# Performance work log

Measured on AMD Instinct MI355X. Metric: run time of the kernel, lower is better.

Reference implementation:

```python
import jax, jax.numpy as jnp
import numpy as np

TOP_K = 2

def setup_inputs() -> dict:
    key = jax.random.key(0)
    ks = jax.random.split(key, 6)
    B, S, D, H, E = 2, 1024, 512, 1024, 8
    x = jax.random.normal(ks[0], (B, S, D), dtype=jnp.float32)
    w_router = jax.random.normal(ks[1], (E, D), dtype=jnp.float32) / np.sqrt(D)
    b_router = jnp.zeros((E,), dtype=jnp.float32)
    w1 = jax.random.normal(ks[2], (E, H, D), dtype=jnp.float32) / np.sqrt(D)   # per-expert fc1 (hidden, in)
    w2 = jax.random.normal(ks[3], (E, D, H), dtype=jnp.float32) / np.sqrt(H)   # per-expert fc2 (out, hidden)
    return {"x": x, "w_router": w_router, "b_router": b_router, "w1": w1, "w2": w2}


def reference(x, w_router, b_router, w1, w2):
    B, S, D = x.shape
    E = w_router.shape[0]
    x_flat = x.reshape(-1, D)                                  # [T, D]
    # Router: logits -> softmax -> top-k -> renormalize -> dispatch weights
    router_logits = x_flat @ w_router.T + b_router             # [T, E]
    probs = jax.nn.softmax(router_logits, axis=-1)
    top_p, top_i = jax.lax.top_k(probs, TOP_K)                 # [T, K]
    top_p = top_p / jnp.sum(top_p, axis=-1, keepdims=True)
    # dispatch[t, e] = normalized prob if e in top-k of t else 0
    dispatch = jnp.sum(jax.nn.one_hot(top_i, E, dtype=x.dtype) * top_p[..., None], axis=1)  # [T, E]
    # Dense-masked expert MLP (mathematically identical to gather/GEMM/scatter):
    h = jax.nn.gelu(jnp.einsum('td,ehd->teh', x_flat, w1), approximate=False)  # [T, E, H]
    y = jnp.einsum('teh,edh->ted', h, w2)                      # [T, E, Dout]
    out = jnp.einsum('ted,te->td', y, dispatch)                # weighted combine
    out = out.reshape(B, S, -1)
    return out, router_logits
```

## Files before the change

kernel.cpp:

```cpp
#include <hip/hip_runtime.h>
#include <hip/hip_bf16.h>
#include <math.h>

#define T_TOK 2048
#define DIM 512
#define HID 1024
#define NE 8
#define CAP 1024

#define ROUT_BLKS 128
#define CAST_BLKS 2048

typedef __attribute__((ext_vector_type(8))) short short8;
typedef __attribute__((ext_vector_type(4))) float floatx4;

__device__ __forceinline__ unsigned short f2bf_bits(float f) {
    __hip_bfloat16 h = __float2bfloat16(f);
    return *reinterpret_cast<unsigned short*>(&h);
}

__device__ __forceinline__ void gl2lds(const unsigned short* g, unsigned short* l) {
    __builtin_amdgcn_global_load_lds(
        (const __attribute__((address_space(1))) unsigned int*)g,
        (__attribute__((address_space(3))) unsigned int*)l, 16, 0, 0);
}

__device__ __forceinline__ short8 frag(const unsigned short* s, int row, int kg) {
    return *reinterpret_cast<const short8*>(s + row * 128 + (((kg) ^ (row & 7)) << 3));
}

template<int T>
__device__ __forceinline__ void stage_tile(const unsigned short* src, size_t RS,
                                           int k0, unsigned short* lds,
                                           int wave, int lane) {
    int ro = lane >> 4, gr = lane & 15;
#pragma unroll
    for (int i = wave; i < T / 4; i += 4) {
        int r = i * 4 + ro;
        gl2lds(src + (size_t)r * RS + k0 + (((gr ^ (r & 7)) << 3)),
               lds + i * 512);
    }
}

__global__ __launch_bounds__(256)
void prep(const float* __restrict__ x, const float* __restrict__ wr,
          const float* __restrict__ br,
          const float* __restrict__ w1, const float* __restrict__ w2,
          unsigned short* __restrict__ w1b, unsigned short* __restrict__ w2b,
          unsigned short* __restrict__ xg, int* __restrict__ counts,
          int2* __restrict__ pairSlot, float2* __restrict__ pw,
          float* __restrict__ logits_out) {
    int bx = blockIdx.x;
    int tid = threadIdx.x;
    if (bx >= ROUT_BLKS) {
        const int n1 = NE * HID * DIM / 4;
        int base = (bx - ROUT_BLKS) * 1024 + tid;
#pragma unroll
        for (int rep = 0; rep < 4; rep++) {
            int i = base + rep * 256;
            const float* s = (i < n1) ? w1 : w2;
            unsigned short* d = (i < n1) ? w1b : w2b;
            int j = (i < n1) ? i : i - n1;
            float4 v = reinterpret_cast<const float4*>(s)[j];
            ushort4 o;
            o.x = f2bf_bits(v.x); o.y = f2bf_bits(v.y);
            o.z = f2bf_bits(v.z); o.w = f2bf_bits(v.w);
            reinterpret_cast<ushort4*>(d)[j] = o;
        }
        return;
    }
    int wave = tid >> 6, lane = tid & 63;
    for (int it = 0; it < 4; it++) {
        int t = bx * 16 + it * 4 + wave;
        const float4* xr = reinterpret_cast<const float4*>(x + (size_t)t * DIM);
        float4 xa = xr[lane * 2], xc = xr[lane * 2 + 1];
        short8 o;
        o[0] = (short)f2bf_bits(xa.x); o[1] = (short)f2bf_bits(xa.y);
        o[2] = (short)f2bf_bits(xa.z); o[3] = (short)f2bf_bits(xa.w);
        o[4] = (short)f2bf_bits(xc.x); o[5] = (short)f2bf_bits(xc.y);
        o[6] = (short)f2bf_bits(xc.z); o[7] = (short)f2bf_bits(xc.w);
        float p[NE];
#pragma unroll
        for (int e = 0; e < NE; e++) {
            const float4* wre = reinterpret_cast<const float4*>(wr + e * DIM);
            float4 wa = wre[lane * 2], wc = wre[lane * 2 + 1];
            p[e] = xa.x * wa.x + xa.y * wa.y + xa.z * wa.z + xa.w * wa.w
                 + xc.x * wc.x + xc.y * wc.y + xc.z * wc.z + xc.w * wc.w;
        }
#pragma unroll
        for (int e = 0; e < NE; e++) {
#pragma unroll
            for (int off = 32; off >= 1; off >>= 1)
                p[e] += __shfl_xor(p[e], off, 64);
        }
        int slot1 = 0, slot2 = 0;
        if (lane == 0) {
            float l[NE];
#pragma unroll
            for (int e = 0; e < NE; e++) {
                l[e] = p[e] + br[e];
                logits_out[(size_t)t * NE + e] = l[e];
            }
            int e1 = 0;
#pragma unroll
            for (int e = 1; e < NE; e++) if (l[e] > l[e1]) e1 = e;
            int es = -1;
#pragma unroll
            for (int e = 0; e < NE; e++) {
                if (e == e1) continue;
                if (es < 0 || l[e] > l[es]) es = e;
            }
            float z = expf(l[es] - l[e1]);
            float inv = 1.f / (1.f + z);
            int pos1 = atomicAdd(&counts[e1 * 16], 1);
            if (pos1 > CAP - 1) pos1 = CAP - 1;
            int pos2 = atomicAdd(&counts[es * 16], 1);
            if (pos2 > CAP - 1) pos2 = CAP - 1;
            slot1 = e1 * CAP + pos1;
            slot2 = es * CAP + pos2;
            pairSlot[t] = make_int2(slot1, slot2);
            pw[t] = make_float2(inv, z * inv);
        }
        slot1 = __shfl(slot1, 0);
        slot2 = __shfl(slot2, 0);
        *reinterpret_cast<short8*>(xg + (size_t)slot1 * DIM + lane * 8) = o;
        *reinterpret_cast<short8*>(xg + (size_t)slot2 * DIM + lane * 8) = o;
    }
}

__global__ __launch_bounds__(256, 3)
void gemm1(const unsigned short* __restrict__ xg,
           const unsigned short* __restrict__ w1b,
           const int* __restrict__ counts,
           unsigned short* __restrict__ Hb) {
    int bx = blockIdx.x;
    int e = bx & 7;
    int rest = bx >> 3;
    int n0 = (rest & 7) * 128;
    int m0 = (rest >> 3) * 64;
    int cnt = counts[e * 16]; if (cnt > CAP) cnt = CAP;
    if (m0 >= cnt) return;

    __shared__ __align__(16) unsigned short s_a[64 * 128];
    __shared__ __align__(16) unsigned short s_b[128 * 128];

    int tid = threadIdx.x, wave = tid >> 6, lane = tid & 63;
    int g = lane >> 4, ln = lane & 15;
    int wm = wave & 1, wn = wave >> 1;

    const unsigned short* asrc = xg + (size_t)(e * CAP + m0) * DIM;
    const unsigned short* bsrc = w1b + (size_t)(e * HID + n0) * DIM;

    floatx4 acc[2][4];
#pragma unroll
    for (int mf = 0; mf < 2; mf++)
#pragma unroll
        for (int nf = 0; nf < 4; nf++) acc[mf][nf] = (floatx4){0.f, 0.f, 0.f, 0.f};

    for (int ph = 0; ph < 4; ph++) {
        int k0 = ph * 128;
        stage_tile<64>(asrc, DIM, k0, s_a, wave, lane);
        stage_tile<128>(bsrc, DIM, k0, s_b, wave, lane);
        __syncthreads();
#pragma unroll
        for (int ks = 0; ks < 4; ks++) {
            short8 a0 = frag(s_a, wm * 32 + ln, ks * 4 + g);
            short8 a1 = frag(s_a, wm * 32 + 16 + ln, ks * 4 + g);
#pragma unroll
            for (int nf = 0; nf < 4; nf++) {
                short8 b = frag(s_b, wn * 64 + nf * 16 + ln, ks * 4 + g);
                acc[0][nf] = __builtin_amdgcn_mfma_f32_16x16x32_bf16(a0, b, acc[0][nf], 0, 0, 0);
                acc[1][nf] = __builtin_amdgcn_mfma_f32_16x16x32_bf16(a1, b, acc[1][nf], 0, 0, 0);
            }
        }
        __syncthreads();
    }
#pragma unroll
    for (int mf = 0; mf < 2; mf++)
#pragma unroll
        for (int nf = 0; nf < 4; nf++)
#pragma unroll
            for (int r = 0; r < 4; r++) {
                int lr = wm * 32 + mf * 16 + g * 4 + r;
                int col = n0 + wn * 64 + nf * 16 + ln;
                float v = acc[mf][nf][r];
                float gv = 0.5f * v * (1.f + erff(v * 0.70710678118f));
                Hb[(size_t)(e * CAP + m0 + lr) * HID + col] = f2bf_bits(gv);
            }
}

__global__ __launch_bounds__(256, 3)
void gemm2(const unsigned short* __restrict__ Hb,
           const unsigned short* __restrict__ w2b,
           const int* __restrict__ counts,
           float* __restrict__ ybuf) {
    int bx = blockIdx.x;
    int e = bx & 7;
    int rest = bx >> 3;
    int n0 = (rest & 3) * 128;
    int kv = (rest >> 2) & 1;
    int m0 = (rest >> 3) * 64;
    int cnt = counts[e * 16]; if (cnt > CAP) cnt = CAP;
    if (m0 >= cnt) return;

    __shared__ __align__(16) unsigned short s_a[64 * 128];
    __shared__ __align__(16) unsigned short s_b[128 * 128];

    int tid = threadIdx.x, wave = tid >> 6, lane = tid & 63;
    int g = lane >> 4, ln = lane & 15;
    int wm = wave & 1, wn = wave >> 1;

    const unsigned short* asrc = Hb + (size_t)(e * CAP + m0) * HID;
    const unsigned short* bsrc = w2b + (size_t)(e * DIM + n0) * HID;

    floatx4 acc[2][4];
#pragma unroll
    for (int mf = 0; mf < 2; mf++)
#pragma unroll
        for (int nf = 0; nf < 4; nf++) acc[mf][nf] = (floatx4){0.f, 0.f, 0.f, 0.f};

    for (int ph = 0; ph < 4; ph++) {
        int k0 = kv * 512 + ph * 128;
        stage_tile<64>(asrc, HID, k0, s_a, wave, lane);
        stage_tile<128>(bsrc, HID, k0, s_b, wave, lane);
        __syncthreads();
#pragma unroll
        for (int ks = 0; ks < 4; ks++) {
            short8 a0 = frag(s_a, wm * 32 + ln, ks * 4 + g);
            short8 a1 = frag(s_a, wm * 32 + 16 + ln, ks * 4 + g);
#pragma unroll
            for (int nf = 0; nf < 4; nf++) {
                short8 b = frag(s_b, wn * 64 + nf * 16 + ln, ks * 4 + g);
                acc[0][nf] = __builtin_amdgcn_mfma_f32_16x16x32_bf16(a0, b, acc[0][nf], 0, 0, 0);
                acc[1][nf] = __builtin_amdgcn_mfma_f32_16x16x32_bf16(a1, b, acc[1][nf], 0, 0, 0);
            }
        }
        __syncthreads();
    }
    float* yb = ybuf + (size_t)kv * (NE * CAP * DIM);
#pragma unroll
    for (int mf = 0; mf < 2; mf++)
#pragma unroll
        for (int nf = 0; nf < 4; nf++)
#pragma unroll
            for (int r = 0; r < 4; r++) {
                int lr = wm * 32 + mf * 16 + g * 4 + r;
                int col = n0 + wn * 64 + nf * 16 + ln;
                yb[(size_t)(e * CAP + m0 + lr) * DIM + col] = acc[mf][nf][r];
            }
}

__global__ __launch_bounds__(256)
void combine_kernel(const float* __restrict__ ybuf, const int2* __restrict__ pairSlot,
                    const float2* __restrict__ pw, float* __restrict__ out) {
    int id = blockIdx.x * 256 + threadIdx.x;
    int t = id >> 7, dv = id & 127;
    int2 s = pairSlot[t];
    float2 w = pw[t];
    const size_t KV = (size_t)NE * CAP * DIM;
    const float4* y0a = reinterpret_cast<const float4*>(ybuf + (size_t)s.x * DIM);
    const float4* y1a = reinterpret_cast<const float4*>(ybuf + KV + (size_t)s.x * DIM);
    const float4* y0b = reinterpret_cast<const float4*>(ybuf + (size_t)s.y * DIM);
    const float4* y1b = reinterpret_cast<const float4*>(ybuf + KV + (size_t)s.y * DIM);
    float4 a = y0a[dv], b = y1a[dv], c = y0b[dv], d = y1b[dv];
    float4 r;
    r.x = w.x * (a.x + b.x) + w.y * (c.x + d.x);
    r.y = w.x * (a.y + b.y) + w.y * (c.y + d.y);
    r.z = w.x * (a.z + b.z) + w.y * (c.z + d.z);
    r.w = w.x * (a.w + b.w) + w.y * (c.w + d.w);
    reinterpret_cast<float4*>(out)[(size_t)t * 128 + dv] = r;
}

extern "C" void kernel_launch(void* const* d_in, const int* in_sizes, int n_in,
                              void* d_out, int out_size, void* d_ws, size_t ws_size,
                              hipStream_t stream) {
    const float* x  = (const float*)d_in[0];
    const float* wr = (const float*)d_in[1];
    const float* br = (const float*)d_in[2];
    const float* w1 = (const float*)d_in[3];
    const float* w2 = (const float*)d_in[4];
    float* out = (float*)d_out;
    float* logits_out = out + (size_t)T_TOK * DIM;

    char* ws = (char*)d_ws;
    int*    counts   = (int*)ws;
    int2*   pairSlot = (int2*)(ws + 4096);
    float2* pw       = (float2*)(ws + 24576);
    unsigned short* xg  = (unsigned short*)(ws + 131072);
    unsigned short* w1b = (unsigned short*)(ws + 8519680);
    unsigned short* w2b = (unsigned short*)(ws + 16908288);
    unsigned short* Hb  = (unsigned short*)(ws + 25296896);
    float*          ybuf = (float*)(ws + 42074112);

    hipMemsetAsync(counts, 0, 512, stream);

    prep<<<ROUT_BLKS + CAST_BLKS, 256, 0, stream>>>(
        x, wr, br, w1, w2, w1b, w2b, xg, counts, pairSlot, pw, logits_out);

    gemm1<<<NE * 16 * 8, 256, 0, stream>>>(xg, w1b, counts, Hb);

    gemm2<<<NE * 16 * 2 * 4, 256, 0, stream>>>(Hb, w2b, counts, ybuf);

    combine_kernel<<<1024, 256, 0, stream>>>(ybuf, pairSlot, pw, out);
}
```

Measured before the change: 126.6 us.

## Fuse router, weight cast, both GEMMs and combine into one persistent kernel with flags

Replaces the four separate kernel launches with a single persistent 512-block kernel. Stages are chained through global atomic counters: per-tile cast-done flags, a router-done count, per-expert-row GEMM1 completion flags and a global GEMM2 counter. This removes launch gaps and lets GEMM work start as soon as the weight tiles it needs are cast. In exchange it depends on every block being co-resident (occupancy of 2 blocks per CU is requested) to avoid deadlock, and it adds spin-wait overhead.

```diff
diff --git a/kernel.cpp b/kernel.cpp
--- a/kernel.cpp
+++ b/kernel.cpp
@@ -7,9 +7,7 @@
 #define HID 1024
 #define NE 8
 #define CAP 1024
-
-#define ROUT_BLKS 128
-#define CAST_BLKS 2048
+#define GRID 512
 
 typedef __attribute__((ext_vector_type(8))) short short8;
 typedef __attribute__((ext_vector_type(4))) float floatx4;
@@ -42,233 +40,254 @@
     }
 }
 
-__global__ __launch_bounds__(256)
-void prep(const float* __restrict__ x, const float* __restrict__ wr,
-          const float* __restrict__ br,
-          const float* __restrict__ w1, const float* __restrict__ w2,
-          unsigned short* __restrict__ w1b, unsigned short* __restrict__ w2b,
-          unsigned short* __restrict__ xg, int* __restrict__ counts,
-          int2* __restrict__ pairSlot, float2* __restrict__ pw,
-          float* __restrict__ logits_out) {
-    int bx = blockIdx.x;
-    int tid = threadIdx.x;
-    if (bx >= ROUT_BLKS) {
-        const int n1 = NE * HID * DIM / 4;
-        int base = (bx - ROUT_BLKS) * 1024 + tid;
-#pragma unroll
-        for (int rep = 0; rep < 4; rep++) {
-            int i = base + rep * 256;
-            const float* s = (i < n1) ? w1 : w2;
-            unsigned short* d = (i < n1) ? w1b : w2b;
-            int j = (i < n1) ? i : i - n1;
-            float4 v = reinterpret_cast<const float4*>(s)[j];
-            ushort4 o;
-            o.x = f2bf_bits(v.x); o.y = f2bf_bits(v.y);
-            o.z = f2bf_bits(v.z); o.w = f2bf_bits(v.w);
-            reinterpret_cast<ushort4*>(d)[j] = o;
-        }
-        return;
-    }
-    int wave = tid >> 6, lane = tid & 63;
-    for (int it = 0; it < 4; it++) {
-        int t = bx * 16 + it * 4 + wave;
-        const float4* xr = reinterpret_cast<const float4*>(x + (size_t)t * DIM);
-        float4 xa = xr[lane * 2], xc = xr[lane * 2 + 1];
-        short8 o;
-        o[0] = (short)f2bf_bits(xa.x); o[1] = (short)f2bf_bits(xa.y);
-        o[2] = (short)f2bf_bits(xa.z); o[3] = (short)f2bf_bits(xa.w);
-        o[4] = (short)f2bf_bits(xc.x); o[5] = (short)f2bf_bits(xc.y);
-        o[6] = (short)f2bf_bits(xc.z); o[7] = (short)f2bf_bits(xc.w);
-        float p[NE];
-#pragma unroll
-        for (int e = 0; e < NE; e++) {
-            const float4* wre = reinterpret_cast<const float4*>(wr + e * DIM);
-            float4 wa = wre[lane * 2], wc = wre[lane * 2 + 1];
-            p[e] = xa.x * wa.x + xa.y * wa.y + xa.z * wa.z + xa.w * wa.w
-                 + xc.x * wc.x + xc.y * wc.y + xc.z * wc.z + xc.w * wc.w;
-        }
-#pragma unroll
-        for (int e = 0; e < NE; e++) {
-#pragma unroll
-            for (int off = 32; off >= 1; off >>= 1)
-                p[e] += __shfl_xor(p[e], off, 64);
-        }
-        int slot1 = 0, slot2 = 0;
-        if (lane == 0) {
-            float l[NE];
-#pragma unroll
-            for (int e = 0; e < NE; e++) {
-                l[e] = p[e] + br[e];
-                logits_out[(size_t)t * NE + e] = l[e];
-            }
-            int e1 = 0;
-#pragma unroll
-            for (int e = 1; e < NE; e++) if (l[e] > l[e1]) e1 = e;
-            int es = -1;
-#pragma unroll
-            for (int e = 0; e < NE; e++) {
-                if (e == e1) continue;
-                if (es < 0 || l[e] > l[es]) es = e;
-            }
-            float z = expf(l[es] - l[e1]);
-            float inv = 1.f / (1.f + z);
-            int pos1 = atomicAdd(&counts[e1 * 16], 1);
-            if (pos1 > CAP - 1) pos1 = CAP - 1;
-            int pos2 = atomicAdd(&counts[es * 16], 1);
-            if (pos2 > CAP - 1) pos2 = CAP - 1;
-            slot1 = e1 * CAP + pos1;
-            slot2 = es * CAP + pos2;
-            pairSlot[t] = make_int2(slot1, slot2);
-            pw[t] = make_float2(inv, z * inv);
-        }
-        slot1 = __shfl(slot1, 0);
-        slot2 = __shfl(slot2, 0);
-        *reinterpret_cast<short8*>(xg + (size_t)slot1 * DIM + lane * 8) = o;
-        *reinterpret_cast<short8*>(xg + (size_t)slot2 * DIM + lane * 8) = o;
-    }
-}
-
-__global__ __launch_bounds__(256, 3)
-void gemm1(const unsigned short* __restrict__ xg,
-           const unsigned short* __restrict__ w1b,
-           const int* __restrict__ counts,
-           unsigned short* __restrict__ Hb) {
-    int bx = blockIdx.x;
-    int e = bx & 7;
-    int rest = bx >> 3;
-    int n0 = (rest & 7) * 128;
-    int m0 = (rest >> 3) * 64;
-    int cnt = counts[e * 16]; if (cnt > CAP) cnt = CAP;
-    if (m0 >= cnt) return;
-
+__device__ __forceinline__ void release_inc(int* flag, int tid) {
+    __syncthreads();
+    if (tid == 0) { __threadfence(); atomicAdd(flag, 1); }
+}
+__device__ __forceinline__ void acquire_wait(int* flag, int target, int tid) {
+    if (tid == 0) {
+        while (atomicAdd(flag, 0) != target) {}
+        __threadfence();
+    }
+    __syncthreads();
+}
+
+__global__ __launch_bounds__(256, 2)
+void moe_mega(const float* __restrict__ x, const float* __restrict__ wr,
+              const float* __restrict__ br, const float* __restrict__ w1,
+              const float* __restrict__ w2,
+              unsigned short* __restrict__ w1b, unsigned short* __restrict__ w2b,
+              unsigned short* __restrict__ xg, int* __restrict__ flags,
+              int2* __restrict__ pairSlot, float2* __restrict__ pw,
+              unsigned short* __restrict__ Hb, float* __restrict__ ybuf,
+              float* __restrict__ out, float* __restrict__ logits_out) {
     __shared__ __align__(16) unsigned short s_a[64 * 128];
     __shared__ __align__(16) unsigned short s_b[128 * 128];
 
-    int tid = threadIdx.x, wave = tid >> 6, lane = tid & 63;
-    int g = lane >> 4, ln = lane & 15;
-    int wm = wave & 1, wn = wave >> 1;
-
-    const unsigned short* asrc = xg + (size_t)(e * CAP + m0) * DIM;
-    const unsigned short* bsrc = w1b + (size_t)(e * HID + n0) * DIM;
-
-    floatx4 acc[2][4];
-#pragma unroll
-    for (int mf = 0; mf < 2; mf++)
-#pragma unroll
-        for (int nf = 0; nf < 4; nf++) acc[mf][nf] = (floatx4){0.f, 0.f, 0.f, 0.f};
-
-    for (int ph = 0; ph < 4; ph++) {
-        int k0 = ph * 128;
-        stage_tile<64>(asrc, DIM, k0, s_a, wave, lane);
-        stage_tile<128>(bsrc, DIM, k0, s_b, wave, lane);
-        __syncthreads();
-#pragma unroll
-        for (int ks = 0; ks < 4; ks++) {
-            short8 a0 = frag(s_a, wm * 32 + ln, ks * 4 + g);
-            short8 a1 = frag(s_a, wm * 32 + 16 + ln, ks * 4 + g);
-#pragma unroll
-            for (int nf = 0; nf < 4; nf++) {
-                short8 b = frag(s_b, wn * 64 + nf * 16 + ln, ks * 4 + g);
-                acc[0][nf] = __builtin_amdgcn_mfma_f32_16x16x32_bf16(a0, b, acc[0][nf], 0, 0, 0);
-                acc[1][nf] = __builtin_amdgcn_mfma_f32_16x16x32_bf16(a1, b, acc[1][nf], 0, 0, 0);
-            }
+    int* counts     = flags;
+    int* routerDone = flags + 256;
+    int* castDone   = flags + 320;
+    int* h1done     = flags + 512;
+    int* g2total    = flags + 640;
+
+    const int bx = blockIdx.x, tid = threadIdx.x;
+    const int wave = tid >> 6, lane = tid & 63;
+    const int g = lane >> 4, ln = lane & 15;
+    const int wm = wave & 1, wn = wave >> 1;
+
+    if (bx < 128) {
+        for (int it = 0; it < 4; it++) {
+            int t = bx * 16 + it * 4 + wave;
+            const float4* xr = reinterpret_cast<const float4*>(x + (size_t)t * DIM);
+            float4 xa = xr[lane * 2], xc = xr[lane * 2 + 1];
+            short8 o;
+            o[0] = (short)f2bf_bits(xa.x); o[1] = (short)f2bf_bits(xa.y);
+            o[2] = (short)f2bf_bits(xa.z); o[3] = (short)f2bf_bits(xa.w);
+            o[4] = (short)f2bf_bits(xc.x); o[5] = (short)f2bf_bits(xc.y);
+            o[6] = (short)f2bf_bits(xc.z); o[7] = (short)f2bf_bits(xc.w);
+            float p[NE];
+#pragma unroll
+            for (int e = 0; e < NE; e++) {
+                const float4* wre = reinterpret_cast<const float4*>(wr + e * DIM);
+                float4 wa = wre[lane * 2], wc = wre[lane * 2 + 1];
+                p[e] = xa.x * wa.x + xa.y * wa.y + xa.z * wa.z + xa.w * wa.w
+                     + xc.x * wc.x + xc.y * wc.y + xc.z * wc.z + xc.w * wc.w;
+            }
+#pragma unroll
+            for (int e = 0; e < NE; e++) {
+#pragma unroll
+                for (int off = 32; off >= 1; off >>= 1)
+                    p[e] += __shfl_xor(p[e], off, 64);
+            }
+            int slot1 = 0, slot2 = 0;
+            if (lane == 0) {
+                float l[NE];
+#pragma unroll
+                for (int e = 0; e < NE; e++) {
+                    l[e] = p[e] + br[e];
+                    logits_out[(size_t)t * NE + e] = l[e];
+                }
+                int e1 = 0;
+#pragma unroll
+                for (int e = 1; e < NE; e++) if (l[e] > l[e1]) e1 = e;
+                int es = -1;
+#pragma unroll
+                for (int e = 0; e < NE; e++) {
+                    if (e == e1) continue;
+                    if (es < 0 || l[e] > l[es]) es = e;
+                }
+                float z = expf(l[es] - l[e1]);
+                float inv = 1.f / (1.f + z);
+                int pos1 = atomicAdd(&counts[e1 * 16], 1);
+                if (pos1 > CAP - 1) pos1 = CAP - 1;
+                int pos2 = atomicAdd(&counts[es * 16], 1);
+                if (pos2 > CAP - 1) pos2 = CAP - 1;
+                slot1 = e1 * CAP + pos1;
+                slot2 = es * CAP + pos2;
+                pairSlot[t] = make_int2(slot1, slot2);
+                pw[t] = make_float2(inv, z * inv);
+            }
+            slot1 = __shfl(slot1, 0);
+            slot2 = __shfl(slot2, 0);
+            *reinterpret_cast<short8*>(xg + (size_t)slot1 * DIM + lane * 8) = o;
+            *reinterpret_cast<short8*>(xg + (size_t)slot2 * DIM + lane * 8) = o;
         }
-        __syncthreads();
-    }
-#pragma unroll
-    for (int mf = 0; mf < 2; mf++)
-#pragma unroll
-        for (int nf = 0; nf < 4; nf++)
-#pragma unroll
-            for (int r = 0; r < 4; r++) {
-                int lr = wm * 32 + mf * 16 + g * 4 + r;
-                int col = n0 + wn * 64 + nf * 16 + ln;
-                float v = acc[mf][nf][r];
-                float gv = 0.5f * v * (1.f + erff(v * 0.70710678118f));
-                Hb[(size_t)(e * CAP + m0 + lr) * HID + col] = f2bf_bits(gv);
-            }
-}
-
-__global__ __launch_bounds__(256, 3)
-void gemm2(const unsigned short* __restrict__ Hb,
-           const unsigned short* __restrict__ w2b,
-           const int* __restrict__ counts,
-           float* __restrict__ ybuf) {
-    int bx = blockIdx.x;
-    int e = bx & 7;
-    int rest = bx >> 3;
-    int n0 = (rest & 3) * 128;
-    int kv = (rest >> 2) & 1;
-    int m0 = (rest >> 3) * 64;
-    int cnt = counts[e * 16]; if (cnt > CAP) cnt = CAP;
-    if (m0 >= cnt) return;
-
-    __shared__ __align__(16) unsigned short s_a[64 * 128];
-    __shared__ __align__(16) unsigned short s_b[128 * 128];
-
-    int tid = threadIdx.x, wave = tid >> 6, lane = tid & 63;
-    int g = lane >> 4, ln = lane & 15;
-    int wm = wave & 1, wn = wave >> 1;
-
-    const unsigned short* asrc = Hb + (size_t)(e * CAP + m0) * HID;
-    const unsigned short* bsrc = w2b + (size_t)(e * DIM + n0) * HID;
-
-    floatx4 acc[2][4];
-#pragma unroll
-    for (int mf = 0; mf < 2; mf++)
-#pragma unroll
-        for (int nf = 0; nf < 4; nf++) acc[mf][nf] = (floatx4){0.f, 0.f, 0.f, 0.f};
-
-    for (int ph = 0; ph < 4; ph++) {
-        int k0 = kv * 512 + ph * 128;
-        stage_tile<64>(asrc, HID, k0, s_a, wave, lane);
-        stage_tile<128>(bsrc, HID, k0, s_b, wave, lane);
-        __syncthreads();
-#pragma unroll
-        for (int ks = 0; ks < 4; ks++) {
-            short8 a0 = frag(s_a, wm * 32 + ln, ks * 4 + g);
-            short8 a1 = frag(s_a, wm * 32 + 16 + ln, ks * 4 + g);
-#pragma unroll
-            for (int nf = 0; nf < 4; nf++) {
-                short8 b = frag(s_b, wn * 64 + nf * 16 + ln, ks * 4 + g);
-                acc[0][nf] = __builtin_amdgcn_mfma_f32_16x16x32_bf16(a0, b, acc[0][nf], 0, 0, 0);
-                acc[1][nf] = __builtin_amdgcn_mfma_f32_16x16x32_bf16(a1, b, acc[1][nf], 0, 0, 0);
+        release_inc(routerDone, tid);
+    } else {
+        int sj = bx - 128;
+        int tile = sj >> 2, q = sj & 3;
+        if (tile < 64) {
+            int e = tile >> 3, ni = tile & 7;
+            size_t base = (size_t)(e * HID + ni * 128 + q * 32) * DIM;
+            const float4* s = reinterpret_cast<const float4*>(w1 + base);
+            ushort4* d = reinterpret_cast<ushort4*>(w1b + base);
+#pragma unroll
+            for (int k = 0; k < 16; k++) {
+                float4 v = s[k * 256 + tid];
+                ushort4 o;
+                o.x = f2bf_bits(v.x); o.y = f2bf_bits(v.y);
+                o.z = f2bf_bits(v.z); o.w = f2bf_bits(v.w);
+                d[k * 256 + tid] = o;
+            }
+        } else {
+            int u = tile - 64;
+            int e = u >> 2, ni = u & 3;
+            size_t base = (size_t)(e * DIM + ni * 128 + q * 32) * HID;
+            const float4* s = reinterpret_cast<const float4*>(w2 + base);
+            ushort4* d = reinterpret_cast<ushort4*>(w2b + base);
+#pragma unroll
+            for (int k = 0; k < 32; k++) {
+                float4 v = s[k * 256 + tid];
+                ushort4 o;
+                o.x = f2bf_bits(v.x); o.y = f2bf_bits(v.y);
+                o.z = f2bf_bits(v.z); o.w = f2bf_bits(v.w);
+                d[k * 256 + tid] = o;
             }
         }
-        __syncthreads();
-    }
-    float* yb = ybuf + (size_t)kv * (NE * CAP * DIM);
-#pragma unroll
-    for (int mf = 0; mf < 2; mf++)
-#pragma unroll
-        for (int nf = 0; nf < 4; nf++)
-#pragma unroll
-            for (int r = 0; r < 4; r++) {
-                int lr = wm * 32 + mf * 16 + g * 4 + r;
-                int col = n0 + wn * 64 + nf * 16 + ln;
-                yb[(size_t)(e * CAP + m0 + lr) * DIM + col] = acc[mf][nf][r];
-            }
-}
-
-__global__ __launch_bounds__(256)
-void combine_kernel(const float* __restrict__ ybuf, const int2* __restrict__ pairSlot,
-                    const float2* __restrict__ pw, float* __restrict__ out) {
-    int id = blockIdx.x * 256 + threadIdx.x;
-    int t = id >> 7, dv = id & 127;
-    int2 s = pairSlot[t];
-    float2 w = pw[t];
+        release_inc(&castDone[tile], tid);
+    }
+
+#pragma unroll
+    for (int rep = 0; rep < 2; rep++) {
+        int job = bx + rep * 512;
+        int e = job & 7, rest = job >> 3;
+        int ni = rest & 7, mi = rest >> 3;
+        acquire_wait(routerDone, 128, tid);
+        acquire_wait(&castDone[e * 8 + ni], 4, tid);
+        int cnt = counts[e * 16]; if (cnt > CAP) cnt = CAP;
+        int m0 = mi * 64, n0 = ni * 128;
+        if (m0 < cnt) {
+            const unsigned short* asrc = xg + (size_t)(e * CAP + m0) * DIM;
+            const unsigned short* bsrc = w1b + (size_t)(e * HID + n0) * DIM;
+            floatx4 acc[2][4];
+#pragma unroll
+            for (int mf = 0; mf < 2; mf++)
+#pragma unroll
+                for (int nf = 0; nf < 4; nf++) acc[mf][nf] = (floatx4){0.f, 0.f, 0.f, 0.f};
+            for (int ph = 0; ph < 4; ph++) {
+                int k0 = ph * 128;
+                stage_tile<64>(asrc, DIM, k0, s_a, wave, lane);
+                stage_tile<128>(bsrc, DIM, k0, s_b, wave, lane);
+                __syncthreads();
+#pragma unroll
+                for (int ks = 0; ks < 4; ks++) {
+                    short8 a0 = frag(s_a, wm * 32 + ln, ks * 4 + g);
+                    short8 a1 = frag(s_a, wm * 32 + 16 + ln, ks * 4 + g);
+#pragma unroll
+                    for (int nf = 0; nf < 4; nf++) {
+                        short8 b = frag(s_b, wn * 64 + nf * 16 + ln, ks * 4 + g);
+                        acc[0][nf] = __builtin_amdgcn_mfma_f32_16x16x32_bf16(a0, b, acc[0][nf], 0, 0, 0);
+                        acc[1][nf] = __builtin_amdgcn_mfma_f32_16x16x32_bf16(a1, b, acc[1][nf], 0, 0, 0);
+                    }
+                }
+                __syncthreads();
+            }
+#pragma unroll
+            for (int mf = 0; mf < 2; mf++)
+#pragma unroll
+                for (int nf = 0; nf < 4; nf++)
+#pragma unroll
+                    for (int r = 0; r < 4; r++) {
+                        int lr = wm * 32 + mf * 16 + g * 4 + r;
+                        int col = n0 + wn * 64 + nf * 16 + ln;
+                        float v = acc[mf][nf][r];
+                        float gv = 0.5f * v * (1.f + erff(v * 0.70710678118f));
+                        Hb[(size_t)(e * CAP + m0 + lr) * HID + col] = f2bf_bits(gv);
+                    }
+        }
+        release_inc(&h1done[e * 16 + mi], tid);
+    }
+
+#pragma unroll
+    for (int rep = 0; rep < 2; rep++) {
+        int job = bx + rep * 512;
+        int e = job & 7, rest = job >> 3;
+        int ni = rest & 3, kv = (rest >> 2) & 1, mi = rest >> 3;
+        acquire_wait(&h1done[e * 16 + mi], 8, tid);
+        acquire_wait(&castDone[64 + e * 4 + ni], 4, tid);
+        int cnt = counts[e * 16]; if (cnt > CAP) cnt = CAP;
+        int m0 = mi * 64, n0 = ni * 128;
+        if (m0 < cnt) {
+            const unsigned short* asrc = Hb + (size_t)(e * CAP + m0) * HID;
+            const unsigned short* bsrc = w2b + (size_t)(e * DIM + n0) * HID;
+            floatx4 acc[2][4];
+#pragma unroll
+            for (int mf = 0; mf < 2; mf++)
+#pragma unroll
+                for (int nf = 0; nf < 4; nf++) acc[mf][nf] = (floatx4){0.f, 0.f, 0.f, 0.f};
+            for (int ph = 0; ph < 4; ph++) {
+                int k0 = kv * 512 + ph * 128;
+                stage_tile<64>(asrc, HID, k0, s_a, wave, lane);
+                stage_tile<128>(bsrc, HID, k0, s_b, wave, lane);
+                __syncthreads();
+#pragma unroll
+                for (int ks = 0; ks < 4; ks++) {
+                    short8 a0 = frag(s_a, wm * 32 + ln, ks * 4 + g);
+                    short8 a1 = frag(s_a, wm * 32 + 16 + ln, ks * 4 + g);
+#pragma unroll
+                    for (int nf = 0; nf < 4; nf++) {
+                        short8 b = frag(s_b, wn * 64 + nf * 16 + ln, ks * 4 + g);
+                        acc[0][nf] = __builtin_amdgcn_mfma_f32_16x16x32_bf16(a0, b, acc[0][nf], 0, 0, 0);
+                        acc[1][nf] = __builtin_amdgcn_mfma_f32_16x16x32_bf16(a1, b, acc[1][nf], 0, 0, 0);
+                    }
+                }
+                __syncthreads();
+            }
+            float* yb = ybuf + (size_t)kv * (NE * CAP * DIM);
+#pragma unroll
+            for (int mf = 0; mf < 2; mf++)
+#pragma unroll
+                for (int nf = 0; nf < 4; nf++)
+#pragma unroll
+                    for (int r = 0; r < 4; r++) {
+                        int lr = wm * 32 + mf * 16 + g * 4 + r;
+                        int col = n0 + wn * 64 + nf * 16 + ln;
+                        yb[(size_t)(e * CAP + m0 + lr) * DIM + col] = acc[mf][nf][r];
+                    }
+        }
+        release_inc(g2total, tid);
+    }
+
+    acquire_wait(g2total, 1024, tid);
     const size_t KV = (size_t)NE * CAP * DIM;
-    const float4* y0a = reinterpret_cast<const float4*>(ybuf + (size_t)s.x * DIM);
-    const float4* y1a = reinterpret_cast<const float4*>(ybuf + KV + (size_t)s.x * DIM);
-    const float4* y0b = reinterpret_cast<const float4*>(ybuf + (size_t)s.y * DIM);
-    const float4* y1b = reinterpret_cast<const float4*>(ybuf + KV + (size_t)s.y * DIM);
-    float4 a = y0a[dv], b = y1a[dv], c = y0b[dv], d = y1b[dv];
-    float4 r;
-    r.x = w.x * (a.x + b.x) + w.y * (c.x + d.x);
-    r.y = w.x * (a.y + b.y) + w.y * (c.y + d.y);
-    r.z = w.x * (a.z + b.z) + w.y * (c.z + d.z);
-    r.w = w.x * (a.w + b.w) + w.y * (c.w + d.w);
-    reinterpret_cast<float4*>(out)[(size_t)t * 128 + dv] = r;
+#pragma unroll
+    for (int rep = 0; rep < 2; rep++) {
+        int id = bx * 512 + rep * 256 + tid;
+        int t = id >> 7, dv = id & 127;
+        int2 s = pairSlot[t];
+        float2 w = pw[t];
+        const float4* y0a = reinterpret_cast<const float4*>(ybuf + (size_t)s.x * DIM);
+        const float4* y1a = reinterpret_cast<const float4*>(ybuf + KV + (size_t)s.x * DIM);
+        const float4* y0b = reinterpret_cast<const float4*>(ybuf + (size_t)s.y * DIM);
+        const float4* y1b = reinterpret_cast<const float4*>(ybuf + KV + (size_t)s.y * DIM);
+        float4 a = y0a[dv], b = y1a[dv], c = y0b[dv], d = y1b[dv];
+        float4 r;
+        r.x = w.x * (a.x + b.x) + w.y * (c.x + d.x);
+        r.y = w.x * (a.y + b.y) + w.y * (c.y + d.y);
+        r.z = w.x * (a.z + b.z) + w.y * (c.z + d.z);
+        r.w = w.x * (a.w + b.w) + w.y * (c.w + d.w);
+        reinterpret_cast<float4*>(out)[(size_t)t * 128 + dv] = r;
+    }
 }
 
 extern "C" void kernel_launch(void* const* d_in, const int* in_sizes, int n_in,
@@ -283,7 +302,7 @@
     float* logits_out = out + (size_t)T_TOK * DIM;
 
     char* ws = (char*)d_ws;
-    int*    counts   = (int*)ws;
+    int*    flags    = (int*)ws;
     int2*   pairSlot = (int2*)(ws + 4096);
     float2* pw       = (float2*)(ws + 24576);
     unsigned short* xg  = (unsigned short*)(ws + 131072);
@@ -292,14 +311,9 @@
     unsigned short* Hb  = (unsigned short*)(ws + 25296896);
     float*          ybuf = (float*)(ws + 42074112);
 
-    hipMemsetAsync(counts, 0, 512, stream);
-
-    prep<<<ROUT_BLKS + CAST_BLKS, 256, 0, stream>>>(
-        x, wr, br, w1, w2, w1b, w2b, xg, counts, pairSlot, pw, logits_out);
-
-    gemm1<<<NE * 16 * 8, 256, 0, stream>>>(xg, w1b, counts, Hb);
-
-    gemm2<<<NE * 16 * 2 * 4, 256, 0, stream>>>(Hb, w2b, counts, ybuf);
-
-    combine_kernel<<<1024, 256, 0, stream>>>(ybuf, pairSlot, pw, out);
-}
+    hipMemsetAsync(flags, 0, 4096, stream);
+
+    moe_mega<<<GRID, 256, 0, stream>>>(x, wr, br, w1, w2, w1b, w2b, xg,
+                                       flags, pairSlot, pw, Hb, ybuf,
+                                       out, logits_out);
+}
```

Measured after the change: 332.6 us. 163% more time.
